# Kernel optimization log

Hardware: AMD Instinct MI355X
Metric: run time of the kernel (lower is better)

Reference implementation:

```python
import jax, jax.numpy as jnp
import numpy as np

B, S, M, D, DI, H, DH, DFF = 2, 1024, 1024, 1024, 1024, 16, 64, 4096
NEG = -1e30


def _ln(x, g, b, eps=1e-5):
    mu = jnp.mean(x, -1, keepdims=True)
    var = jnp.mean((x - mu) ** 2, -1, keepdims=True)
    return (x - mu) / jnp.sqrt(var + eps) * g + b


def _rel_shift(x):
    # x: (b, i, j, h) -- Transformer-XL shift via pad + reshape (exact torch trick)
    b, i, j, h = x.shape
    zp = jnp.zeros((b, 1, j, h), x.dtype)
    xp = jnp.concatenate([zp, x], axis=1).reshape(i + 1, b, j, h)
    return xp[1:].reshape(b, i, j, h)


def setup_inputs() -> dict:
    key = jax.random.key(0)
    ks = jax.random.split(key, 24)
    rn = lambda k, sh, s=1.0: jax.random.normal(k, sh, jnp.float32) * s
    St = S + M
    causal = jnp.arange(St)[None, :] > (jnp.arange(S)[:, None] + M)  # (S, St)
    tgt_mask = jnp.broadcast_to(causal[None, :, :, None], (B, S, St, 1))
    return {
        "x": rn(ks[0], (B, S, D)),
        "enc_output": rn(ks[1], (B, S, D)),
        "pos_emb": rn(ks[2], (St, DI)),
        "u": rn(ks[3], (H, DH), 0.02),
        "v": rn(ks[4], (H, DH), 0.02),
        "mem": rn(ks[5], (B, M, D)),
        "tgt_mask": tgt_mask,
        "Wq_m": rn(ks[6], (D, DI), 0.02),
        "Wkv_m": rn(ks[7], (D, 2 * DI), 0.02),
        "fcw_m": rn(ks[8], (DI, D), 0.02),
        "fcb_m": jnp.zeros((D,), jnp.float32),
        "lnm_g": jnp.ones((D,), jnp.float32),
        "lnm_b": jnp.zeros((D,), jnp.float32),
        "Wq_c": rn(ks[9], (D, DI), 0.02),
        "Wkv_c": rn(ks[10], (D, 2 * DI), 0.02),
        "fcw_c": rn(ks[11], (DI, D), 0.02),
        "fcb_c": jnp.zeros((D,), jnp.float32),
        "lnc_g": jnp.ones((D,), jnp.float32),
        "lnc_b": jnp.zeros((D,), jnp.float32),
        "W1": rn(ks[12], (D, DFF), 0.02),
        "b1": jnp.zeros((DFF,), jnp.float32),
        "W2": rn(ks[13], (DFF, D), 0.02),
        "b2": jnp.zeros((D,), jnp.float32),
        "ln1_g": jnp.ones((D,), jnp.float32),
        "ln1_b": jnp.zeros((D,), jnp.float32),
        "ln2_g": jnp.ones((D,), jnp.float32),
        "ln2_b": jnp.zeros((D,), jnp.float32),
        "ln3_g": jnp.ones((D,), jnp.float32),
        "ln3_b": jnp.zeros((D,), jnp.float32),
    }


def reference(x, enc_output, pos_emb, u, v, mem, tgt_mask,
              Wq_m, Wkv_m, fcw_m, fcb_m, lnm_g, lnm_b,
              Wq_c, Wkv_c, fcw_c, fcb_c, lnc_g, lnc_b,
              W1, b1, W2, b2,
              ln1_g, ln1_b, ln2_g, ln2_b, ln3_g, ln3_b):
    scale = 1.0 / (DH ** 0.5)

    def mha(xn):  # RecurrenceAttention (internal post-norm, pre_norm=False)
        h = jnp.concatenate([mem, xn], axis=1)                       # (B, M+S, D)
        q = (xn @ Wq_m).reshape(B, S, H, DH)
        k, vv = jnp.split(h @ Wkv_m, 2, axis=-1)
        k = k.reshape(B, S + M, H, DH)
        vv = vv.reshape(B, S + M, H, DH)
        content = jnp.einsum('bihd,bjhd->bijh', q + u, k)
        pe = pos_emb.reshape(S + M, H, DH)
        pos = jnp.einsum('bihd,jhd->bijh', q + v, pe)
        attn = content + _rel_shift(pos)
        attn = jnp.where(tgt_mask, NEG, attn)
        attn = attn * scale
        attn = jax.nn.softmax(attn, axis=1)                          # NOTE: query axis (faithful)
        o = jnp.einsum('bijh,bjhd->bihd', attn, vv).reshape(B, S, DI)
        return _ln(xn + o @ fcw_m + fcb_m, lnm_g, lnm_b)

    def cross(dec):  # CrossAttention (internal post-norm)
        q = (dec @ Wq_c).reshape(B, S, H, DH)
        k, vv = jnp.split(enc_output @ Wkv_c, 2, axis=-1)
        k = k.reshape(B, S, H, DH)
        vv = vv.reshape(B, S, H, DH)
        attn = jnp.einsum('bihd,bjhd->bijh', q, k) * scale
        attn = jax.nn.softmax(attn, axis=1)                          # query axis (faithful)
        o = jnp.einsum('bijh,bjhd->bihd', attn, vv).reshape(B, S, DI)
        return _ln(dec + o @ fcw_c + fcb_c, lnc_g, lnc_b)

    # decoder layer, pre_norm=True path
    out = x + mha(_ln(x, ln1_g, ln1_b))
    out2 = out + cross(_ln(out, ln2_g, ln2_b))
    h = jax.nn.gelu(_ln(out2, ln3_g, ln3_b) @ W1 + b1, approximate=False)
    out3 = out2 + (h @ W2 + b2)
    return out3
```

## Files before the change

### kernel.cpp

```cpp
#include <hip/hip_runtime.h>

typedef unsigned short u16;
typedef __attribute__((ext_vector_type(4))) unsigned short u16x4;
typedef __attribute__((ext_vector_type(8))) unsigned short u16x8;
typedef __attribute__((ext_vector_type(8))) __bf16 bf16x8;
typedef __attribute__((ext_vector_type(4))) float f32x4;

#define DEV __device__ __forceinline__

DEV float b2f(u16 u){ union{ unsigned int i; float f; } x; x.i = ((unsigned int)u) << 16; return x.f; }
DEV u16 f2b(float f){ unsigned int x = __float_as_uint(f); return (u16)((x + 0x7fffu + ((x >> 16) & 1u)) >> 16); }

DEV void block_red2(float& s, float& q){
#pragma unroll
  for (int off = 32; off; off >>= 1){ s += __shfl_down(s, off); q += __shfl_down(q, off); }
  __shared__ float sh1[4], sh2[4];
  int lane = threadIdx.x & 63, w = threadIdx.x >> 6;
  if (lane == 0){ sh1[w] = s; sh2[w] = q; }
  __syncthreads();
  s = sh1[0] + sh1[1] + sh1[2] + sh1[3];
  q = sh2[0] + sh2[1] + sh2[2] + sh2[3];
}

template<int WM, int WN, bool OUTB>
__global__ __launch_bounds__(WM*WN*64) void gemm_bt(
    const u16* __restrict__ A, const u16* __restrict__ Bm, void* __restrict__ Cp,
    int K, int lda, int ldb, int ldc, int Hh,
    long aob, long aoh, long bob, long boh, long cob, long coh)
{
  constexpr int BM = WM*64, BN = WN*64, BK = 64, NW = WM*WN;
  __shared__ u16 At[BM*64];
  __shared__ u16 Bt[BN*64];
  int z = blockIdx.z, b_ = z / Hh, h_ = z % Hh;
  const u16* Ab = A + (long)b_*aob + (long)h_*aoh;
  const u16* Bb = Bm + (long)b_*bob + (long)h_*boh;
  long cbase = (long)b_*cob + (long)h_*coh;
  int m0 = blockIdx.y * BM, n0 = blockIdx.x * BN;
  int tid = threadIdx.x, lane = tid & 63, wv = tid >> 6;
  int wm = wv / WN, wn = wv % WN;
  f32x4 acc[4][4];
  f32x4 z4 = {0.f, 0.f, 0.f, 0.f};
#pragma unroll
  for (int a = 0; a < 4; a++)
#pragma unroll
    for (int b = 0; b < 4; b++) acc[a][b] = z4;
  int lr = lane & 15, lk8 = (lane >> 4) * 8;
  int rq = lane >> 3, cq = (lane & 7) << 3;
  for (int k0 = 0; k0 < K; k0 += BK){
    __syncthreads();
#pragma unroll
    for (int q = wv; q < BM/8; q += NW){
      const u16* g = &Ab[(long)(m0 + q*8 + rq)*lda + k0 + cq];
      __builtin_amdgcn_global_load_lds((const __attribute__((address_space(1))) void*)g,
          (__attribute__((address_space(3))) void*)&At[q*512], 16, 0, 0);
    }
#pragma unroll
    for (int q = wv; q < BN/8; q += NW){
      const u16* g = &Bb[(long)(n0 + q*8 + rq)*ldb + k0 + cq];
      __builtin_amdgcn_global_load_lds((const __attribute__((address_space(1))) void*)g,
          (__attribute__((address_space(3))) void*)&Bt[q*512], 16, 0, 0);
    }
    __syncthreads();
#pragma unroll
    for (int kk = 0; kk < BK; kk += 32){
      bf16x8 af[4], bfr[4];
#pragma unroll
      for (int mi = 0; mi < 4; mi++) af[mi]  = *(bf16x8*)&At[(wm*64 + mi*16 + lr)*64 + kk + lk8];
#pragma unroll
      for (int ni = 0; ni < 4; ni++) bfr[ni] = *(bf16x8*)&Bt[(wn*64 + ni*16 + lr)*64 + kk + lk8];
#pragma unroll
      for (int mi = 0; mi < 4; mi++)
#pragma unroll
        for (int ni = 0; ni < 4; ni++)
          acc[mi][ni] = __builtin_amdgcn_mfma_f32_16x16x32_bf16(af[mi], bfr[ni], acc[mi][ni], 0, 0, 0);
    }
  }
  int orow = (lane >> 4) * 4, ocol = lane & 15;
#pragma unroll
  for (int mi = 0; mi < 4; mi++)
#pragma unroll
    for (int ni = 0; ni < 4; ni++){
      int row = m0 + wm*64 + mi*16 + orow;
      int col = n0 + wn*64 + ni*16 + ocol;
      long cidx = cbase + (long)row*ldc + col;
#pragma unroll
      for (int r = 0; r < 4; r++){
        float vv = acc[mi][ni][r];
        if (OUTB) ((u16*)Cp)[cidx + (long)r*ldc] = f2b(vv);
        else      ((float*)Cp)[cidx + (long)r*ldc] = vv;
      }
    }
}

template<int KD, bool MASK>
__global__ __launch_bounds__(256) void attn_passA(
    const u16* __restrict__ Kp, const u16* __restrict__ Qp, float* __restrict__ mz,
    int J, int kld, int qld,
    long kob, long koh, long qob, long qoh, int H, float scale, int mztot)
{
  constexpr int KP = KD + 8;
  __shared__ u16 Qt[128*KP];
  int bh = blockIdx.y, b = bh / H, h = bh % H;
  const u16* Kb = Kp + (long)b*kob + (long)h*koh;
  const u16* Qb = Qp + (long)b*qob + (long)h*qoh;
  int j0 = blockIdx.x * 64;
  int tid = threadIdx.x, lane = tid & 63, w = tid >> 6;
  int lr = lane & 15, lk8 = (lane >> 4) * 8;
  constexpr int RCH = KD / 8;
  bf16x8 ak[KD/32];
  {
    const u16* kr = &Kb[(long)(j0 + w*16 + lr)*kld];
#pragma unroll
    for (int kk = 0; kk < KD/32; kk++) ak[kk] = *(const bf16x8*)&kr[kk*32 + lk8];
  }
  float m_run[4], z_run[4];
#pragma unroll
  for (int r = 0; r < 4; r++){ m_run[r] = -3.0e38f; z_run[r] = 0.f; }
  f32x4 zz = {0.f,0.f,0.f,0.f};
  for (int it = 0; it < 8; it++){
    if (MASK && (it*128 + 127 < j0 - 1024)) continue;
    __syncthreads();
    for (int idx = tid; idx < 128*RCH; idx += 256){
      int r = idx / RCH, c = (idx % RCH) * 8;
      *(u16x8*)&Qt[r*KP + c] = *(const u16x8*)&Qb[(long)(it*128 + r)*qld + c];
    }
    __syncthreads();
    f32x4 acc[8];
#pragma unroll
    for (int ni = 0; ni < 8; ni++) acc[ni] = zz;
#pragma unroll
    for (int kk = 0; kk < KD; kk += 32){
      bf16x8 bq[8];
#pragma unroll
      for (int ni = 0; ni < 8; ni++) bq[ni] = *(bf16x8*)&Qt[(ni*16 + lr)*KP + kk + lk8];
#pragma unroll
      for (int ni = 0; ni < 8; ni++)
        acc[ni] = __builtin_amdgcn_mfma_f32_16x16x32_bf16(ak[kk/32], bq[ni], acc[ni], 0, 0, 0);
    }
#pragma unroll
    for (int r = 0; r < 4; r++){
      int jg = j0 + w*16 + ((lane >> 4) << 2) + r;
      float sv[8]; float tm = -3.0e38f;
#pragma unroll
      for (int ni = 0; ni < 8; ni++){
        int ig = it*128 + ni*16 + (lane & 15);
        float s = acc[ni][r] * scale;
        bool val = (!MASK) || (ig >= jg - 1024);
        sv[ni] = val ? s : -3.0e38f;
        tm = fmaxf(tm, sv[ni]);
      }
#pragma unroll
      for (int off = 1; off < 16; off <<= 1) tm = fmaxf(tm, __shfl_xor(tm, off));
      float mn = fmaxf(m_run[r], tm);
      float zt = 0.f;
#pragma unroll
      for (int ni = 0; ni < 8; ni++)
        zt += (sv[ni] > -1.0e37f) ? __expf(sv[ni] - mn) : 0.f;
#pragma unroll
      for (int off = 1; off < 16; off <<= 1) zt += __shfl_xor(zt, off);
      z_run[r] = z_run[r] * __expf(m_run[r] - mn) + zt;
      m_run[r] = mn;
    }
  }
  if ((lane & 15) == 0){
#pragma unroll
    for (int r = 0; r < 4; r++){
      int jg = j0 + w*16 + ((lane >> 4) << 2) + r;
      mz[(long)bh*J + jg] = m_run[r];
      mz[(long)mztot + (long)bh*J + jg] = 1.f / z_run[r];
    }
  }
}

template<int KD, bool MASK>
__global__ __launch_bounds__(256) void attn_passB(
    const u16* __restrict__ Kp, const u16* __restrict__ Qp, const u16* __restrict__ Vtp,
    const float* __restrict__ mz, float* __restrict__ Op,
    int J, int kld, int qld, int vld, int oldd,
    long kob, long koh, long qob, long qoh, long vob, long voh, long oob, long ooh,
    int H, float scale, int mztot, int jtHalf, long opstride)
{
  constexpr int KP = KD + 8, PSTR = 140, VSTR = 136;
  __shared__ u16 PK[128*KP];
  __shared__ u16 Vtt[64*VSTR];
  u16* Kt = PK;
  u16* Pt = PK;
  int bh = blockIdx.y, b = bh / H, h = bh % H;
  int jh = blockIdx.z;
  const u16* Kb = Kp + (long)b*kob + (long)h*koh;
  const u16* Qb = Qp + (long)b*qob + (long)h*qoh;
  const u16* Vb = Vtp + (long)b*vob + (long)h*voh;
  float* Ob = Op + (long)jh*opstride + (long)b*oob + (long)h*ooh;
  const float* mzm = mz + (long)bh*J;
  const float* mzz = mz + (long)mztot + (long)bh*J;
  int i0 = blockIdx.x * 64;
  int tid = threadIdx.x, lane = tid & 63, w = tid >> 6;
  int lr = lane & 15, lk8 = (lane >> 4) * 8;
  constexpr int RCH = KD / 8;
  bf16x8 aq[KD/32];
  {
    const u16* qr = &Qb[(long)(i0 + w*16 + lr)*qld];
#pragma unroll
    for (int kk = 0; kk < KD/32; kk++) aq[kk] = *(const bf16x8*)&qr[kk*32 + lk8];
  }
  f32x4 acc_o[4];
  f32x4 zz = {0.f,0.f,0.f,0.f};
#pragma unroll
  for (int nd = 0; nd < 4; nd++) acc_o[nd] = zz;
  int jt1 = (jh + 1) * jtHalf;
  for (int jt = jh * jtHalf; jt < jt1; jt++){
    if (MASK && (jt*128 > i0 + 1087)) continue;
    __syncthreads();
    for (int idx = tid; idx < 128*RCH; idx += 256){
      int r = idx / RCH, c = (idx % RCH) * 8;
      *(u16x8*)&Kt[r*KP + c] = *(const u16x8*)&Kb[(long)(jt*128 + r)*kld + c];
    }
    for (int idx = tid; idx < 64*16; idx += 256){
      int r = idx >> 4, c = (idx & 15) << 3;
      *(u16x8*)&Vtt[r*VSTR + c] = *(const u16x8*)&Vb[(long)r*vld + jt*128 + c];
    }
    __syncthreads();
    f32x4 acc[8];
#pragma unroll
    for (int ni = 0; ni < 8; ni++) acc[ni] = zz;
#pragma unroll
    for (int kk = 0; kk < KD; kk += 32){
      bf16x8 bk[8];
#pragma unroll
      for (int ni = 0; ni < 8; ni++) bk[ni] = *(bf16x8*)&Kt[(ni*16 + lr)*KP + kk + lk8];
#pragma unroll
      for (int ni = 0; ni < 8; ni++)
        acc[ni] = __builtin_amdgcn_mfma_f32_16x16x32_bf16(aq[kk/32], bk[ni], acc[ni], 0, 0, 0);
    }
    __syncthreads();
#pragma unroll
    for (int ni = 0; ni < 8; ni++){
      int jg = jt*128 + ni*16 + (lane & 15);
      float mj = mzm[jg], zj = mzz[jg];
#pragma unroll
      for (int r = 0; r < 4; r++){
        int ig = i0 + w*16 + ((lane >> 4) << 2) + r;
        bool val = (!MASK) || (ig >= jg - 1024);
        float p = val ? __expf(acc[ni][r] * scale - mj) * zj : 0.f;
        Pt[(w*16 + ((lane >> 4) << 2) + r)*PSTR + ni*16 + (lane & 15)] = f2b(p);
      }
    }
#pragma unroll
    for (int kk = 0; kk < 128; kk += 32){
      bf16x8 pa, vb[4];
      pa = *(bf16x8*)&Pt[(w*16 + lr)*PSTR + kk + lk8];
#pragma unroll
      for (int nd = 0; nd < 4; nd++) vb[nd] = *(bf16x8*)&Vtt[(nd*16 + lr)*VSTR + kk + lk8];
#pragma unroll
      for (int nd = 0; nd < 4; nd++)
        acc_o[nd] = __builtin_amdgcn_mfma_f32_16x16x32_bf16(pa, vb[nd], acc_o[nd], 0, 0, 0);
    }
  }
#pragma unroll
  for (int nd = 0; nd < 4; nd++)
#pragma unroll
    for (int r = 0; r < 4; r++){
      int ig = i0 + w*16 + ((lane >> 4) << 2) + r;
      int d = nd*16 + (lane & 15);
      Ob[(long)ig*oldd + d] = acc_o[nd][r];
    }
}

__global__ __launch_bounds__(256) void combine_o(const float* __restrict__ p, u16* __restrict__ o)
{
  const long PS = 2097152;
  long i = ((long)blockIdx.x*256 + threadIdx.x) * 4;
  const float* a = &p[i];
  const float* b = &p[i + PS];
  u16x4 r;
#pragma unroll
  for (int e = 0; e < 4; e++) r[e] = f2b(a[e] + b[e]);
  *(u16x4*)&o[i] = r;
}

__global__ __launch_bounds__(256) void transpose_k(
    const u16* __restrict__ src, u16* __restrict__ dst,
    int lds_, int ldd, int Hh, long sob, long soh, long dob, long doh)
{
  __shared__ u16 tile[64*72];
  int z = blockIdx.z, b_ = z / Hh, h_ = z % Hh;
  const u16* S_ = src + (long)b_*sob + (long)h_*soh;
  u16* D_ = dst + (long)b_*dob + (long)h_*doh;
  int r0 = blockIdx.y * 64, c0 = blockIdx.x * 64;
  int tid = threadIdx.x;
  for (int idx = tid; idx < 512; idx += 256){
    int r = idx >> 3, c = (idx & 7) << 3;
    *(u16x8*)&tile[r*72 + c] = *(const u16x8*)&S_[(long)(r0 + r)*lds_ + c0 + c];
  }
  __syncthreads();
  for (int idx = tid; idx < 512; idx += 256){
    int c = idx >> 3, r = (idx & 7) << 3;
    u16x8 v;
#pragma unroll
    for (int e = 0; e < 8; e++) v[e] = tile[(r + e)*72 + c];
    *(u16x8*)&D_[(long)(c0 + c)*ldd + r0 + r] = v;
  }
}

__global__ __launch_bounds__(256) void transpose_cvt_k(
    const float* __restrict__ src, u16* __restrict__ dst, int lds_, int ldd)
{
  __shared__ u16 tile[64*72];
  int r0 = blockIdx.y * 64, c0 = blockIdx.x * 64;
  int tid = threadIdx.x;
  for (int idx = tid; idx < 512; idx += 256){
    int r = idx >> 3, c = (idx & 7) << 3;
    const float* s = &src[(long)(r0 + r)*lds_ + c0 + c];
#pragma unroll
    for (int e = 0; e < 8; e++) tile[r*72 + c + e] = f2b(s[e]);
  }
  __syncthreads();
  for (int idx = tid; idx < 512; idx += 256){
    int c = idx >> 3, r = (idx & 7) << 3;
    u16x8 v;
#pragma unroll
    for (int e = 0; e < 8; e++) v[e] = tile[(r + e)*72 + c];
    *(u16x8*)&dst[(long)(c0 + c)*ldd + r0 + r] = v;
  }
}

__global__ __launch_bounds__(256) void cvt_k(const float* __restrict__ src, u16* __restrict__ dst)
{
  long i = ((long)blockIdx.x*256 + threadIdx.x) * 4;
  float4 v = *(const float4*)&src[i];
  u16x4 o; o[0] = f2b(v.x); o[1] = f2b(v.y); o[2] = f2b(v.z); o[3] = f2b(v.w);
  *(u16x4*)&dst[i] = o;
}

__global__ __launch_bounds__(256) void ln_k(const float* __restrict__ src, const float* __restrict__ g,
                                            const float* __restrict__ be, u16* __restrict__ out)
{
  long base = (long)blockIdx.x * 1024;
  int tid = threadIdx.x;
  const float* s = src + base + tid*4;
  float v[4] = {s[0], s[1], s[2], s[3]};
  float s1 = v[0]+v[1]+v[2]+v[3];
  float s2 = v[0]*v[0]+v[1]*v[1]+v[2]*v[2]+v[3]*v[3];
  block_red2(s1, s2);
  float mu = s1 * (1.f/1024.f);
  float var = s2 * (1.f/1024.f) - mu*mu;
  float rs = rsqrtf(var + 1e-5f);
#pragma unroll
  for (int e = 0; e < 4; e++){
    int col = tid*4 + e;
    out[base + col] = f2b((v[e]-mu)*rs*g[col] + be[col]);
  }
}

__global__ __launch_bounds__(256) void add_ln_k(const float* __restrict__ go,
    const u16* __restrict__ xn, const float* __restrict__ bias,
    const float* __restrict__ g, const float* __restrict__ be,
    const float* __restrict__ resid, float* __restrict__ outp)
{
  const long PS = 2097152;
  long base = (long)blockIdx.x * 1024;
  int tid = threadIdx.x;
  float v[4];
#pragma unroll
  for (int e = 0; e < 4; e++){
    int col = tid*4 + e;
    long idx = base + col;
    v[e] = go[idx] + go[idx + PS] + go[idx + 2*PS] + go[idx + 3*PS] + b2f(xn[idx]) + bias[col];
  }
  float s1 = v[0]+v[1]+v[2]+v[3];
  float s2 = v[0]*v[0]+v[1]*v[1]+v[2]*v[2]+v[3]*v[3];
  block_red2(s1, s2);
  float mu = s1 * (1.f/1024.f);
  float var = s2 * (1.f/1024.f) - mu*mu;
  float rs = rsqrtf(var + 1e-5f);
#pragma unroll
  for (int e = 0; e < 4; e++){
    int col = tid*4 + e;
    outp[base + col] = resid[base + col] + (v[e]-mu)*rs*g[col] + be[col];
  }
}

__global__ __launch_bounds__(256) void build_qq(const u16* __restrict__ q, const float* __restrict__ u,
                                                const float* __restrict__ v, u16* __restrict__ QQ)
{
  int bi = blockIdx.x;
  long qrow = (long)bi * 1024;
  long obase = (long)bi * 2048;
  int n = bi + 2;
  int bp = n / 1025, ip = n % 1025;
  long qsrc = ip ? ((long)(bp*1024 + ip - 1)) * 1024 : -1;
  for (int t = threadIdx.x; t < 2048; t += 256){
    int h = t >> 7, e = t & 127;
    float val;
    if (e < 64) val = b2f(q[qrow + h*64 + e]) + u[h*64 + e];
    else {
      int d = e - 64;
      val = (qsrc < 0) ? 0.f : b2f(q[qsrc + h*64 + d]) + v[h*64 + d];
    }
    QQ[obase + t] = f2b(val);
  }
}

__global__ __launch_bounds__(256) void build_bb(const u16* __restrict__ kv, const float* __restrict__ pe,
                                                u16* __restrict__ BB)
{
  int bj = blockIdx.x;
  int j = bj & 2047;
  long kvrow = (long)bj * 2048;
  long obase = (long)bj * 2048;
  for (int t = threadIdx.x; t < 2048; t += 256){
    int h = t >> 7, e = t & 127;
    u16 val = (e < 64) ? kv[kvrow + h*64 + e] : f2b(pe[(long)j*1024 + h*64 + (e - 64)]);
    BB[obase + t] = val;
  }
}

__global__ __launch_bounds__(256) void gelu_k(const float* __restrict__ f1, const float* __restrict__ b1,
                                              u16* __restrict__ h1)
{
  long i = (long)blockIdx.x*256 + threadIdx.x;
  float x = f1[i] + b1[i & 4095];
  h1[i] = f2b(0.5f * x * (1.f + erff(x * 0.70710678118654752f)));
}

__global__ __launch_bounds__(256) void final_k(const float* __restrict__ out2, const float* __restrict__ f2,
                                               const float* __restrict__ b2v, float* __restrict__ outp)
{
  const long PS = 2097152;
  long i = (long)blockIdx.x*256 + threadIdx.x;
  outp[i] = out2[i] + f2[i] + f2[i + PS] + f2[i + 2*PS] + f2[i + 3*PS] + b2v[i & 1023];
}

extern "C" void kernel_launch(void* const* d_in, const int* in_sizes, int n_in,
                              void* d_out, int out_size, void* d_ws, size_t ws_size,
                              hipStream_t stream)
{
  (void)in_sizes; (void)n_in; (void)out_size; (void)ws_size;
  const float* X    = (const float*)d_in[0];
  const float* ENC  = (const float*)d_in[1];
  const float* PE   = (const float*)d_in[2];
  const float* Uu   = (const float*)d_in[3];
  const float* Vv   = (const float*)d_in[4];
  const float* MEM  = (const float*)d_in[5];
  const float* WQM  = (const float*)d_in[7];
  const float* WKVM = (const float*)d_in[8];
  const float* FCWM = (const float*)d_in[9];
  const float* FCBM = (const float*)d_in[10];
  const float* LNMG = (const float*)d_in[11];
  const float* LNMB = (const float*)d_in[12];
  const float* WQC  = (const float*)d_in[13];
  const float* WKVC = (const float*)d_in[14];
  const float* FCWC = (const float*)d_in[15];
  const float* FCBC = (const float*)d_in[16];
  const float* LNCG = (const float*)d_in[17];
  const float* LNCB = (const float*)d_in[18];
  const float* W1   = (const float*)d_in[19];
  const float* B1   = (const float*)d_in[20];
  const float* W2   = (const float*)d_in[21];
  const float* B2   = (const float*)d_in[22];
  const float* LN1G = (const float*)d_in[23];
  const float* LN1B = (const float*)d_in[24];
  const float* LN2G = (const float*)d_in[25];
  const float* LN2B = (const float*)d_in[26];
  const float* LN3G = (const float*)d_in[27];
  const float* LN3B = (const float*)d_in[28];
  float* OUT = (float*)d_out;
  char* W = (char*)d_ws;
  const size_t MB = 1ull << 20;

  u16*   wT_a  = (u16*)(W + 0*MB);
  u16*   wT_b  = (u16*)(W + 2*MB);
  u16*   wT_c  = (u16*)(W + 6*MB);
  u16*   w1T   = (u16*)(W + 0*MB);
  u16*   xn1   = (u16*)(W + 8*MB);
  u16*   q     = (u16*)(W + 12*MB);
  u16*   o_b   = (u16*)(W + 12*MB);
  u16*   kv    = (u16*)(W + 16*MB);
  float* outb  = (float*)(W + 24*MB);
  u16*   QQ    = (u16*)(W + 32*MB);
  u16*   xn2   = (u16*)(W + 32*MB);
  u16*   qc    = (u16*)(W + 36*MB);
  u16*   BB    = (u16*)(W + 40*MB);
  u16*   kvc   = (u16*)(W + 40*MB);
  u16*   Vtc   = (u16*)(W + 48*MB);
  u16*   oc    = (u16*)(W + 52*MB);
  u16*   Vt    = (u16*)(W + 56*MB);
  u16*   w2T   = (u16*)(W + 56*MB);
  float* mzb   = (float*)(W + 64*MB);
  u16*   memb  = (u16*)(W + 68*MB);
  u16*   encb  = (u16*)(W + 68*MB);
  float* opart = (float*)(W + 66*MB);
  float* ofc   = (float*)(W + 66*MB);
  float* f1    = (float*)(W + 66*MB);
  float* f2    = (float*)(W + 66*MB);
  u16*   h1    = (u16*)(W + 98*MB);
  float* out2b = (float*)(W + 114*MB);

  transpose_cvt_k<<<dim3(16,16),256,0,stream>>>(WQM,  wT_a, 1024,1024);
  transpose_cvt_k<<<dim3(32,16),256,0,stream>>>(WKVM, wT_b, 2048,1024);
  transpose_cvt_k<<<dim3(16,16),256,0,stream>>>(FCWM, wT_c, 1024,1024);
  cvt_k<<<2048,256,0,stream>>>(MEM, memb);
  ln_k<<<2048,256,0,stream>>>(X, LN1G, LN1B, xn1);
  gemm_bt<2,2,true><<<dim3(8,16,1),256,0,stream>>>(xn1, wT_a, q, 1024, 1024,1024,1024, 1, 0,0,0,0,0,0);
  gemm_bt<2,2,true><<<dim3(16,8,2),256,0,stream>>>(memb, wT_b, kv, 1024, 1024,1024,2048, 1,
      1048576,0, 0,0, 4194304,0);
  gemm_bt<2,2,true><<<dim3(16,8,2),256,0,stream>>>(xn1, wT_b, kv + (size_t)1024*2048, 1024, 1024,1024,2048, 1,
      1048576,0, 0,0, 4194304,0);
  build_qq<<<2048,256,0,stream>>>(q, Uu, Vv, QQ);
  build_bb<<<4096,256,0,stream>>>(kv, PE, BB);
  transpose_k<<<dim3(1,32,32),256,0,stream>>>(kv + 1024, Vt, 2048, 2048, 16,
      4194304,64, 2097152,131072);
  attn_passA<128,true><<<dim3(32,32),256,0,stream>>>(BB, QQ, mzb, 2048, 2048, 2048,
      4194304,128, 2097152,128, 16, 0.125f, 65536);
  attn_passB<128,true><<<dim3(16,32,2),256,0,stream>>>(BB, QQ, Vt, mzb, opart, 2048,
      2048,2048,2048,1024, 4194304,128, 2097152,128, 2097152,131072, 1048576,64, 16, 0.125f, 65536,
      8, 2097152);
  combine_o<<<2048,256,0,stream>>>(opart, o_b);
  gemm_bt<2,2,false><<<dim3(8,16,4),256,0,stream>>>(o_b, wT_c, ofc, 256, 1024,1024,1024, 4,
      0,256, 0,256, 0,2097152);
  add_ln_k<<<2048,256,0,stream>>>(ofc, xn1, FCBM, LNMG, LNMB, X, outb);

  transpose_cvt_k<<<dim3(16,16),256,0,stream>>>(WQC,  wT_a, 1024,1024);
  transpose_cvt_k<<<dim3(32,16),256,0,stream>>>(WKVC, wT_b, 2048,1024);
  transpose_cvt_k<<<dim3(16,16),256,0,stream>>>(FCWC, wT_c, 1024,1024);
  cvt_k<<<2048,256,0,stream>>>(ENC, encb);
  ln_k<<<2048,256,0,stream>>>(outb, LN2G, LN2B, xn2);
  gemm_bt<2,2,true><<<dim3(8,16,1),256,0,stream>>>(xn2, wT_a, qc, 1024, 1024,1024,1024, 1, 0,0,0,0,0,0);
  gemm_bt<2,2,true><<<dim3(16,16,1),256,0,stream>>>(encb, wT_b, kvc, 1024, 1024,1024,2048, 1, 0,0,0,0,0,0);
  transpose_k<<<dim3(1,16,32),256,0,stream>>>(kvc + 1024, Vtc, 2048, 1024, 16,
      2097152,64, 1048576,65536);
  attn_passA<64,false><<<dim3(16,32),256,0,stream>>>(kvc, qc, mzb, 1024, 2048, 1024,
      2097152,64, 1048576,64, 16, 0.125f, 32768);
  attn_passB<64,false><<<dim3(16,32,2),256,0,stream>>>(kvc, qc, Vtc, mzb, opart, 1024,
      2048,1024,1024,1024, 2097152,64, 1048576,64, 1048576,65536, 1048576,64, 16, 0.125f, 32768,
      4, 2097152);
  combine_o<<<2048,256,0,stream>>>(opart, oc);
  gemm_bt<2,2,false><<<dim3(8,16,4),256,0,stream>>>(oc, wT_c, ofc, 256, 1024,1024,1024, 4,
      0,256, 0,256, 0,2097152);
  add_ln_k<<<2048,256,0,stream>>>(ofc, xn2, FCBC, LNCG, LNCB, outb, out2b);

  transpose_cvt_k<<<dim3(64,16),256,0,stream>>>(W1, w1T, 4096,1024);
  transpose_cvt_k<<<dim3(16,64),256,0,stream>>>(W2, w2T, 1024,4096);
  ln_k<<<2048,256,0,stream>>>(out2b, LN3G, LN3B, xn2);
  gemm_bt<2,2,false><<<dim3(32,16,1),256,0,stream>>>(xn2, w1T, f1, 1024, 1024,1024,4096, 1, 0,0,0,0,0,0);
  gelu_k<<<32768,256,0,stream>>>(f1, B1, h1);
  gemm_bt<2,2,false><<<dim3(8,16,4),256,0,stream>>>(h1, w2T, f2, 1024, 4096,4096,1024, 4,
      0,1024, 0,1024, 0,2097152);
  final_k<<<8192,256,0,stream>>>(out2b, f2, B2, OUT);
}
```

Measured before the change: 733.0 us.

## Register-prefetch next Q/K/V tiles in attention passes to overlap global loads

Both attention passes now load the next tile of Q (pass A) or K and V (pass B) from global memory into registers while the current tile is processed, then store it to shared memory at the top of the next iteration. Loop bounds for masked tiles are computed up front instead of using continue checks, and the per-tile softmax stats are loaded before the QK MFMA loop. The aim is to hide global load latency behind compute. The cost is extra register pressure from the prefetch buffers, which may reduce occupancy.

```diff
diff --git a/kernel.cpp b/kernel.cpp
--- a/kernel.cpp
+++ b/kernel.cpp
@@ -99,6 +99,8 @@
     long kob, long koh, long qob, long qoh, int H, float scale, int mztot)
 {
   constexpr int KP = KD + 8;
+  constexpr int RCH = KD / 8;
+  constexpr int QREG = KD / 16;
   __shared__ u16 Qt[128*KP];
   int bh = blockIdx.y, b = bh / H, h = bh % H;
   const u16* Kb = Kp + (long)b*kob + (long)h*koh;
@@ -106,7 +108,6 @@
   int j0 = blockIdx.x * 64;
   int tid = threadIdx.x, lane = tid & 63, w = tid >> 6;
   int lr = lane & 15, lk8 = (lane >> 4) * 8;
-  constexpr int RCH = KD / 8;
   bf16x8 ak[KD/32];
   {
     const u16* kr = &Kb[(long)(j0 + w*16 + lr)*kld];
@@ -117,12 +118,27 @@
 #pragma unroll
   for (int r = 0; r < 4; r++){ m_run[r] = -3.0e38f; z_run[r] = 0.f; }
   f32x4 zz = {0.f,0.f,0.f,0.f};
-  for (int it = 0; it < 8; it++){
-    if (MASK && (it*128 + 127 < j0 - 1024)) continue;
+  int itLo = 0;
+  if (MASK){ int tt = j0 - 1151; itLo = tt > 0 ? (tt + 127)/128 : 0; }
+  u16x8 qreg[QREG];
+#pragma unroll
+  for (int qq = 0; qq < QREG; qq++){
+    int idx = tid + qq*256; int r = idx / RCH, c = (idx % RCH) * 8;
+    qreg[qq] = *(const u16x8*)&Qb[(long)(itLo*128 + r)*qld + c];
+  }
+  for (int it = itLo; it < 8; it++){
     __syncthreads();
-    for (int idx = tid; idx < 128*RCH; idx += 256){
-      int r = idx / RCH, c = (idx % RCH) * 8;
-      *(u16x8*)&Qt[r*KP + c] = *(const u16x8*)&Qb[(long)(it*128 + r)*qld + c];
+#pragma unroll
+    for (int qq = 0; qq < QREG; qq++){
+      int idx = tid + qq*256; int r = idx / RCH, c = (idx % RCH) * 8;
+      *(u16x8*)&Qt[r*KP + c] = qreg[qq];
+    }
+    if (it + 1 < 8){
+#pragma unroll
+      for (int qq = 0; qq < QREG; qq++){
+        int idx = tid + qq*256; int r = idx / RCH, c = (idx % RCH) * 8;
+        qreg[qq] = *(const u16x8*)&Qb[(long)((it+1)*128 + r)*qld + c];
+      }
     }
     __syncthreads();
     f32x4 acc[8];
@@ -181,6 +197,8 @@
     int H, float scale, int mztot, int jtHalf, long opstride)
 {
   constexpr int KP = KD + 8, PSTR = 140, VSTR = 136;
+  constexpr int RCH = KD / 8;
+  constexpr int KREG = KD / 16;
   __shared__ u16 PK[128*KP];
   __shared__ u16 Vtt[64*VSTR];
   u16* Kt = PK;
@@ -196,7 +214,6 @@
   int i0 = blockIdx.x * 64;
   int tid = threadIdx.x, lane = tid & 63, w = tid >> 6;
   int lr = lane & 15, lk8 = (lane >> 4) * 8;
-  constexpr int RCH = KD / 8;
   bf16x8 aq[KD/32];
   {
     const u16* qr = &Qb[(long)(i0 + w*16 + lr)*qld];
@@ -207,53 +224,86 @@
   f32x4 zz = {0.f,0.f,0.f,0.f};
 #pragma unroll
   for (int nd = 0; nd < 4; nd++) acc_o[nd] = zz;
-  int jt1 = (jh + 1) * jtHalf;
-  for (int jt = jh * jtHalf; jt < jt1; jt++){
-    if (MASK && (jt*128 > i0 + 1087)) continue;
-    __syncthreads();
-    for (int idx = tid; idx < 128*RCH; idx += 256){
-      int r = idx / RCH, c = (idx % RCH) * 8;
-      *(u16x8*)&Kt[r*KP + c] = *(const u16x8*)&Kb[(long)(jt*128 + r)*kld + c];
-    }
-    for (int idx = tid; idx < 64*16; idx += 256){
-      int r = idx >> 4, c = (idx & 15) << 3;
-      *(u16x8*)&Vtt[r*VSTR + c] = *(const u16x8*)&Vb[(long)r*vld + jt*128 + c];
-    }
-    __syncthreads();
-    f32x4 acc[8];
-#pragma unroll
-    for (int ni = 0; ni < 8; ni++) acc[ni] = zz;
-#pragma unroll
-    for (int kk = 0; kk < KD; kk += 32){
-      bf16x8 bk[8];
-#pragma unroll
-      for (int ni = 0; ni < 8; ni++) bk[ni] = *(bf16x8*)&Kt[(ni*16 + lr)*KP + kk + lk8];
-#pragma unroll
-      for (int ni = 0; ni < 8; ni++)
-        acc[ni] = __builtin_amdgcn_mfma_f32_16x16x32_bf16(aq[kk/32], bk[ni], acc[ni], 0, 0, 0);
-    }
-    __syncthreads();
-#pragma unroll
-    for (int ni = 0; ni < 8; ni++){
-      int jg = jt*128 + ni*16 + (lane & 15);
-      float mj = mzm[jg], zj = mzz[jg];
-#pragma unroll
-      for (int r = 0; r < 4; r++){
-        int ig = i0 + w*16 + ((lane >> 4) << 2) + r;
-        bool val = (!MASK) || (ig >= jg - 1024);
-        float p = val ? __expf(acc[ni][r] * scale - mj) * zj : 0.f;
-        Pt[(w*16 + ((lane >> 4) << 2) + r)*PSTR + ni*16 + (lane & 15)] = f2b(p);
-      }
-    }
-#pragma unroll
-    for (int kk = 0; kk < 128; kk += 32){
-      bf16x8 pa, vb[4];
-      pa = *(bf16x8*)&Pt[(w*16 + lr)*PSTR + kk + lk8];
-#pragma unroll
-      for (int nd = 0; nd < 4; nd++) vb[nd] = *(bf16x8*)&Vtt[(nd*16 + lr)*VSTR + kk + lk8];
-#pragma unroll
-      for (int nd = 0; nd < 4; nd++)
-        acc_o[nd] = __builtin_amdgcn_mfma_f32_16x16x32_bf16(pa, vb[nd], acc_o[nd], 0, 0, 0);
+  int lo = jh * jtHalf, hi = lo + jtHalf;
+  if (MASK){ int lim = (i0 + 1087)/128 + 1; hi = hi < lim ? hi : lim; }
+  if (lo < hi){
+    u16x8 kreg[KREG];
+    u16x8 vreg[4];
+#pragma unroll
+    for (int qq = 0; qq < KREG; qq++){
+      int idx = tid + qq*256; int r = idx / RCH, c = (idx % RCH) * 8;
+      kreg[qq] = *(const u16x8*)&Kb[(long)(lo*128 + r)*kld + c];
+    }
+#pragma unroll
+    for (int qq = 0; qq < 4; qq++){
+      int idx = tid + qq*256; int r = idx >> 4, c = (idx & 15) << 3;
+      vreg[qq] = *(const u16x8*)&Vb[(long)r*vld + lo*128 + c];
+    }
+    for (int jt = lo; jt < hi; jt++){
+      __syncthreads();
+#pragma unroll
+      for (int qq = 0; qq < KREG; qq++){
+        int idx = tid + qq*256; int r = idx / RCH, c = (idx % RCH) * 8;
+        *(u16x8*)&Kt[r*KP + c] = kreg[qq];
+      }
+#pragma unroll
+      for (int qq = 0; qq < 4; qq++){
+        int idx = tid + qq*256; int r = idx >> 4, c = (idx & 15) << 3;
+        *(u16x8*)&Vtt[r*VSTR + c] = vreg[qq];
+      }
+      if (jt + 1 < hi){
+#pragma unroll
+        for (int qq = 0; qq < KREG; qq++){
+          int idx = tid + qq*256; int r = idx / RCH, c = (idx % RCH) * 8;
+          kreg[qq] = *(const u16x8*)&Kb[(long)((jt+1)*128 + r)*kld + c];
+        }
+#pragma unroll
+        for (int qq = 0; qq < 4; qq++){
+          int idx = tid + qq*256; int r = idx >> 4, c = (idx & 15) << 3;
+          vreg[qq] = *(const u16x8*)&Vb[(long)r*vld + (jt+1)*128 + c];
+        }
+      }
+      __syncthreads();
+      float mjv[8], zjv[8];
+#pragma unroll
+      for (int ni = 0; ni < 8; ni++){
+        int jg = jt*128 + ni*16 + (lane & 15);
+        mjv[ni] = mzm[jg]; zjv[ni] = mzz[jg];
+      }
+      f32x4 acc[8];
+#pragma unroll
+      for (int ni = 0; ni < 8; ni++) acc[ni] = zz;
+#pragma unroll
+      for (int kk = 0; kk < KD; kk += 32){
+        bf16x8 bk[8];
+#pragma unroll
+        for (int ni = 0; ni < 8; ni++) bk[ni] = *(bf16x8*)&Kt[(ni*16 + lr)*KP + kk + lk8];
+#pragma unroll
+        for (int ni = 0; ni < 8; ni++)
+          acc[ni] = __builtin_amdgcn_mfma_f32_16x16x32_bf16(aq[kk/32], bk[ni], acc[ni], 0, 0, 0);
+      }
+      __syncthreads();
+#pragma unroll
+      for (int ni = 0; ni < 8; ni++){
+        int jg = jt*128 + ni*16 + (lane & 15);
+#pragma unroll
+        for (int r = 0; r < 4; r++){
+          int ig = i0 + w*16 + ((lane >> 4) << 2) + r;
+          bool val = (!MASK) || (ig >= jg - 1024);
+          float p = val ? __expf(acc[ni][r] * scale - mjv[ni]) * zjv[ni] : 0.f;
+          Pt[(w*16 + ((lane >> 4) << 2) + r)*PSTR + ni*16 + (lane & 15)] = f2b(p);
+        }
+      }
+#pragma unroll
+      for (int kk = 0; kk < 128; kk += 32){
+        bf16x8 pa, vb[4];
+        pa = *(bf16x8*)&Pt[(w*16 + lr)*PSTR + kk + lk8];
+#pragma unroll
+        for (int nd = 0; nd < 4; nd++) vb[nd] = *(bf16x8*)&Vtt[(nd*16 + lr)*VSTR + kk + lk8];
+#pragma unroll
+        for (int nd = 0; nd < 4; nd++)
+          acc_o[nd] = __builtin_amdgcn_mfma_f32_16x16x32_bf16(pa, vb[nd], acc_o[nd], 0, 0, 0);
+      }
     }
   }
 #pragma unroll
```

New measurement: 676.3 us. 1.08x faster.
